# Performance work log

Measured on AMD Instinct MI355X. Metric: run time of the kernel, lower is better.

## Reference

```python
import jax, jax.numpy as jnp
import numpy as np

B, S, D, H = 2, 2048, 1024, 16
DK = D // H

def setup_inputs() -> dict:
    key = jax.random.key(0)
    ks = jax.random.split(key, 12)
    inp = {
        'Q': jax.random.normal(ks[0], (B, S, D), jnp.float32),
        'K': jax.random.normal(ks[1], (B, S, D), jnp.float32),
        'V': jax.random.normal(ks[2], (B, S, D), jnp.float32),
        # causal mask broadcast over batch/heads; masked_fill where mask==0
        'mask': jnp.tril(jnp.ones((1, 1, S, S), jnp.int32)),
        'Wq': jax.random.normal(ks[3], (D, D), jnp.float32) / np.sqrt(D),
        'bq': jnp.zeros((D,), jnp.float32),
        'Wk': jax.random.normal(ks[4], (D, D), jnp.float32) / np.sqrt(D),
        'bk': jnp.zeros((D,), jnp.float32),
        'Wv': jax.random.normal(ks[5], (D, D), jnp.float32) / np.sqrt(D),
        'bv': jnp.zeros((D,), jnp.float32),
        'Wo': jax.random.normal(ks[6], (D, D), jnp.float32) / np.sqrt(D),
        'bo': jnp.zeros((D,), jnp.float32),
    }
    return inp

def _split(x):
    # [B,S,D] -> [B,H,S,DK]
    return x.reshape(B, S, H, DK).transpose(0, 2, 1, 3)

def reference(Q, K, V, mask, Wq, bq, Wk, bk, Wv, bv, Wo, bo):
    q = _split(Q @ Wq.T + bq)
    k = _split(K @ Wk.T + bk)
    v = _split(V @ Wv.T + bv)
    score = jnp.einsum('bhqd,bhkd->bhqk', q, k) / jnp.sqrt(jnp.float32(DK))
    score = jnp.where(mask == 0, jnp.float32(-1e9), score)
    attn = jax.nn.softmax(score, axis=-1)  # dropout is identity at eval
    ctx = jnp.einsum('bhqk,bhkd->bhqd', attn, v)
    out = ctx.transpose(0, 2, 1, 3).reshape(B, S, D)
    return out @ Wo.T + bo
```

## Files before the change

### kernel.cpp

```cpp
#include <hip/hip_runtime.h>

#define B_  2
#define S_  2048
#define D_  1024
#define H_  16
#define DK_ 64

using bf16x8 = __attribute__((ext_vector_type(8))) short;
using f32x4  = __attribute__((ext_vector_type(4))) float;

__device__ __forceinline__ unsigned short f2bf(float f) {
    unsigned u = __builtin_bit_cast(unsigned, f);
    u += 0x7FFFu + ((u >> 16) & 1u);
    return (unsigned short)(u >> 16);
}

__device__ __forceinline__ void gload_lds16(const unsigned short* gsrc, unsigned short* ldst) {
    __builtin_amdgcn_global_load_lds((const __attribute__((address_space(1))) void*)gsrc,
                                     (__attribute__((address_space(3))) void*)ldst, 16, 0, 0);
}

__global__ __launch_bounds__(256) void cast_all_k(
    const float* __restrict__ Q, const float* __restrict__ K, const float* __restrict__ V,
    const float* __restrict__ Wq, const float* __restrict__ Wk, const float* __restrict__ Wv,
    const float* __restrict__ Wo, unsigned short* __restrict__ dst) {
    unsigned gid  = blockIdx.x * 256u + threadIdx.x;
    unsigned base = gid * 4u;
    unsigned seg  = base >> 20;
    const float* src; unsigned off;
    if      (seg <  4u) { src = Q;  off = base; }
    else if (seg <  8u) { src = K;  off = base - (4u  << 20); }
    else if (seg < 12u) { src = V;  off = base - (8u  << 20); }
    else if (seg == 12u){ src = Wq; off = base - (12u << 20); }
    else if (seg == 13u){ src = Wk; off = base - (13u << 20); }
    else if (seg == 14u){ src = Wv; off = base - (14u << 20); }
    else                { src = Wo; off = base - (15u << 20); }
    float4 v = *reinterpret_cast<const float4*>(src + off);
    ushort4 o;
    o.x = f2bf(v.x); o.y = f2bf(v.y); o.z = f2bf(v.z); o.w = f2bf(v.w);
    *reinterpret_cast<ushort4*>(dst + base) = o;
}

__device__ __forceinline__ void gemm_stage(
    const unsigned short* __restrict__ A, const unsigned short* __restrict__ Bm,
    int bm, int bn, int kt, unsigned short* As, unsigned short* Bs, int tid, int w) {
    #pragma unroll
    for (int is = 0; is < 2; ++is) {
        int g = is * 256 + tid;
        int row = g >> 2, c = g & 3;
        gload_lds16(A  + (unsigned)(bm * 128 + row) * 1024 + kt + c * 8,
                    As + (unsigned)(is * 256 + w * 64) * 8);
        gload_lds16(Bm + (unsigned)(bn * 128 + row) * 1024 + kt + c * 8,
                    Bs + (unsigned)(is * 256 + w * 64) * 8);
    }
}

__device__ __forceinline__ void gemm_core(
    const unsigned short* __restrict__ A, const unsigned short* __restrict__ Bm,
    int bm, int bn, f32x4 acc[4][4],
    unsigned short (&As)[2][128 * 32], unsigned short (&Bs)[2][128 * 32]) {
    const int tid = threadIdx.x;
    const int w = tid >> 6, l = tid & 63, lg = l >> 4, lr = l & 15;
    const int wr = w >> 1, wc = w & 1;
    gemm_stage(A, Bm, bm, bn, 0, As[0], Bs[0], tid, w);
    __syncthreads();
    for (int ks = 0; ks < 32; ++ks) {
        const int cur = ks & 1;
        if (ks + 1 < 32)
            gemm_stage(A, Bm, bm, bn, (ks + 1) * 32, As[cur ^ 1], Bs[cur ^ 1], tid, w);
        bf16x8 af[4], bfr[4];
        #pragma unroll
        for (int i = 0; i < 4; ++i)
            af[i]  = *reinterpret_cast<const bf16x8*>(&As[cur][(wr * 64 + i * 16 + lr) * 32 + lg * 8]);
        #pragma unroll
        for (int j = 0; j < 4; ++j)
            bfr[j] = *reinterpret_cast<const bf16x8*>(&Bs[cur][(wc * 64 + j * 16 + lr) * 32 + lg * 8]);
        #pragma unroll
        for (int i = 0; i < 4; ++i)
            #pragma unroll
            for (int j = 0; j < 4; ++j)
                acc[i][j] = __builtin_amdgcn_mfma_f32_16x16x32_bf16(af[i], bfr[j], acc[i][j], 0, 0, 0);
        __syncthreads();
    }
}

__global__ __launch_bounds__(256) void proj_fused_k(
    const unsigned short* __restrict__ bfall,
    const float* __restrict__ bq, const float* __restrict__ bk, const float* __restrict__ bv,
    unsigned short* __restrict__ qh, unsigned short* __restrict__ kh,
    unsigned short* __restrict__ vt) {
    __shared__ __align__(16) unsigned short As[2][128 * 32], Bs[2][128 * 32];
    const unsigned M1 = 1u << 20;
    int bid = blockIdx.x;
    int z = bid >> 8, r = bid & 255;
    const unsigned short *A, *Bm; const float* bias; unsigned short* outp;
    int bm, bn;
    if (z == 0)      { A = bfall;           Bm = bfall + 12 * M1; bias = bq; outp = qh; bm = r >> 3; bn = r & 7; }
    else if (z == 1) { A = bfall + 4 * M1;  Bm = bfall + 13 * M1; bias = bk; outp = kh; bm = r >> 3; bn = r & 7; }
    else             { A = bfall + 14 * M1; Bm = bfall + 8 * M1;  bias = bv; outp = vt; bm = r >> 5; bn = r & 31; }

    f32x4 acc[4][4] = {};
    gemm_core(A, Bm, bm, bn, acc, As, Bs);

    const int tid = threadIdx.x;
    const int w = tid >> 6, l = tid & 63, lg = l >> 4, lr = l & 15;
    const int wr = w >> 1, wc = w & 1;
    #pragma unroll
    for (int i = 0; i < 4; ++i) {
        #pragma unroll
        for (int j = 0; j < 4; ++j) {
            int n = bn * 128 + wc * 64 + j * 16 + lr;
            #pragma unroll
            for (int rr = 0; rr < 4; ++rr) {
                int m = bm * 128 + wr * 64 + i * 16 + 4 * lg + rr;
                float v = acc[i][j][rr];
                if (z < 2) {
                    v += bias[n];
                    if (z == 0) v *= 0.125f;
                    int b = m >> 11, s = m & 2047, h = n >> 6, d = n & 63;
                    outp[(((unsigned)(b * 16 + h) * 2048 + s) << 6) + d] = f2bf(v);
                } else {
                    v += bias[m];
                    int h = m >> 6, d = m & 63, b = n >> 11, s = n & 2047;
                    outp[(((unsigned)(b * 16 + h) << 6) + d) * 2048 + s] = f2bf(v);
                }
            }
        }
    }
}

__device__ __forceinline__ void attn_stage(
    const unsigned short* __restrict__ khb, const unsigned short* __restrict__ vtb,
    int kb, unsigned short* KtB, unsigned short* VtB, int tid, int w) {
    #pragma unroll
    for (int is = 0; is < 2; ++is) {
        int g = is * 256 + tid;
        int row = g >> 3, cp = g & 7;
        int ck = cp ^ (row & 7);
        gload_lds16(khb + (unsigned)(kb + row) * 64 + ck * 8,
                    KtB + (unsigned)(is * 256 + w * 64) * 8);
        gload_lds16(vtb + (unsigned)row * S_ + kb + ck * 8,
                    VtB + (unsigned)(is * 256 + w * 64) * 8);
    }
}

__global__ __launch_bounds__(256) void attn_k(
    const unsigned short* __restrict__ qh, const unsigned short* __restrict__ kh,
    const unsigned short* __restrict__ vt, unsigned short* __restrict__ ctx) {
    __shared__ __align__(16) unsigned short Kt[2][64 * 64], Vt[2][64 * 64], Pb[4][16 * 64];
    const int bh = blockIdx.x, qi = blockIdx.y;
    const int b = bh >> 4, h = bh & 15;
    const int qb = (S_ - 64) - 64 * qi;
    const int tid = threadIdx.x, w = tid >> 6, l = tid & 63, lg = l >> 4, lr = l & 15;
    const unsigned short* khb = kh + (unsigned)bh * S_ * 64;
    const unsigned short* vtb = vt + (unsigned)bh * 64 * S_;

    const unsigned short* qrow = qh + ((unsigned)bh * S_ + qb + w * 16 + lr) * 64 + lg * 8;
    const bf16x8 aq0 = *reinterpret_cast<const bf16x8*>(qrow);
    const bf16x8 aq1 = *reinterpret_cast<const bf16x8*>(qrow + 32);

    f32x4 o[4] = {};
    float m_r[4], l_r[4];
    #pragma unroll
    for (int rr = 0; rr < 4; ++rr) { m_r[rr] = -1e30f; l_r[rr] = 0.f; }

    const int ntiles = qb / 64 + 1;
    attn_stage(khb, vtb, 0, Kt[0], Vt[0], tid, w);
    __syncthreads();
    for (int t = 0; t < ntiles; ++t) {
        const int cur = t & 1;
        if (t + 1 < ntiles)
            attn_stage(khb, vtb, (t + 1) * 64, Kt[cur ^ 1], Vt[cur ^ 1], tid, w);
        const unsigned short* Kc = Kt[cur];
        const unsigned short* Vc = Vt[cur];

        f32x4 sf[4];
        __builtin_amdgcn_s_setprio(1);
        #pragma unroll
        for (int f = 0; f < 4; ++f) {
            f32x4 a = {};
            int row0 = f * 16 + lr;
            bf16x8 bk0 = *reinterpret_cast<const bf16x8*>(&Kc[row0 * 64 + ((lg + 0) ^ (row0 & 7)) * 8]);
            a = __builtin_amdgcn_mfma_f32_16x16x32_bf16(aq0, bk0, a, 0, 0, 0);
            bf16x8 bk1 = *reinterpret_cast<const bf16x8*>(&Kc[row0 * 64 + ((lg + 4) ^ (row0 & 7)) * 8]);
            a = __builtin_amdgcn_mfma_f32_16x16x32_bf16(aq1, bk1, a, 0, 0, 0);
            sf[f] = a;
        }
        __builtin_amdgcn_s_setprio(0);
        const bool diag = (t == ntiles - 1);
        float sc[4];
        #pragma unroll
        for (int rr = 0; rr < 4; ++rr) {
            float mv = -1e30f;
            #pragma unroll
            for (int f = 0; f < 4; ++f) {
                float v = sf[f][rr];
                if (diag && (f * 16 + lr) > (w * 16 + 4 * lg + rr)) v = -1e30f;
                sf[f][rr] = v;
                mv = fmaxf(mv, v);
            }
            mv = fmaxf(mv, __shfl_xor(mv, 1));
            mv = fmaxf(mv, __shfl_xor(mv, 2));
            mv = fmaxf(mv, __shfl_xor(mv, 4));
            mv = fmaxf(mv, __shfl_xor(mv, 8));
            float mn = fmaxf(m_r[rr], mv);
            sc[rr] = __expf(m_r[rr] - mn);
            m_r[rr] = mn;
            float s = 0.f;
            #pragma unroll
            for (int f = 0; f < 4; ++f) {
                float p = __expf(sf[f][rr] - mn);
                sf[f][rr] = p;
                s += p;
            }
            s += __shfl_xor(s, 1); s += __shfl_xor(s, 2);
            s += __shfl_xor(s, 4); s += __shfl_xor(s, 8);
            l_r[rr] = l_r[rr] * sc[rr] + s;
        }
        #pragma unroll
        for (int f2 = 0; f2 < 4; ++f2)
            #pragma unroll
            for (int rr = 0; rr < 4; ++rr)
                o[f2][rr] *= sc[rr];

        unsigned short* Pw = &Pb[w][0];
        #pragma unroll
        for (int f = 0; f < 4; ++f) {
            int col = f * 16 + lr, ch = col >> 3, wi = col & 7;
            #pragma unroll
            for (int rr = 0; rr < 4; ++rr) {
                int row = 4 * lg + rr;
                Pw[row * 64 + ((ch ^ (row & 7)) << 3) + wi] = f2bf(sf[f][rr]);
            }
        }
        asm volatile("s_waitcnt lgkmcnt(0)" ::: "memory");
        bf16x8 ap0 = *reinterpret_cast<const bf16x8*>(&Pw[lr * 64 + ((lg + 0) ^ (lr & 7)) * 8]);
        bf16x8 ap1 = *reinterpret_cast<const bf16x8*>(&Pw[lr * 64 + ((lg + 4) ^ (lr & 7)) * 8]);

        __builtin_amdgcn_s_setprio(1);
        #pragma unroll
        for (int f2 = 0; f2 < 4; ++f2) {
            int row = f2 * 16 + lr;
            bf16x8 bv0 = *reinterpret_cast<const bf16x8*>(&Vc[row * 64 + ((lg + 0) ^ (row & 7)) * 8]);
            o[f2] = __builtin_amdgcn_mfma_f32_16x16x32_bf16(ap0, bv0, o[f2], 0, 0, 0);
            bf16x8 bv1 = *reinterpret_cast<const bf16x8*>(&Vc[row * 64 + ((lg + 4) ^ (row & 7)) * 8]);
            o[f2] = __builtin_amdgcn_mfma_f32_16x16x32_bf16(ap1, bv1, o[f2], 0, 0, 0);
        }
        __builtin_amdgcn_s_setprio(0);
        __syncthreads();
    }

    #pragma unroll
    for (int f2 = 0; f2 < 4; ++f2) {
        #pragma unroll
        for (int rr = 0; rr < 4; ++rr) {
            int s = qb + w * 16 + 4 * lg + rr;
            float v = o[f2][rr] / l_r[rr];
            ctx[(((unsigned)(b * S_ + s) * H_ + h) << 6) + f2 * 16 + lr] = f2bf(v);
        }
    }
}

__global__ __launch_bounds__(256) void final_k(
    const unsigned short* __restrict__ ctx, const unsigned short* __restrict__ Wob,
    const float* __restrict__ bo, float* __restrict__ out) {
    __shared__ __align__(16) unsigned short As[2][128 * 32], Bs[2][128 * 32];
    int bid = blockIdx.x;
    int bm = bid >> 3, bn = bid & 7;
    f32x4 acc[4][4] = {};
    gemm_core(ctx, Wob, bm, bn, acc, As, Bs);
    const int tid = threadIdx.x;
    const int w = tid >> 6, l = tid & 63, lg = l >> 4, lr = l & 15;
    const int wr = w >> 1, wc = w & 1;
    #pragma unroll
    for (int i = 0; i < 4; ++i) {
        #pragma unroll
        for (int j = 0; j < 4; ++j) {
            int n = bn * 128 + wc * 64 + j * 16 + lr;
            float bn_v = bo[n];
            #pragma unroll
            for (int rr = 0; rr < 4; ++rr) {
                int m = bm * 128 + wr * 64 + i * 16 + 4 * lg + rr;
                out[(unsigned)m * 1024 + n] = acc[i][j][rr] + bn_v;
            }
        }
    }
}

extern "C" void kernel_launch(void* const* d_in, const int* in_sizes, int n_in,
                              void* d_out, int out_size, void* d_ws, size_t ws_size,
                              hipStream_t stream) {
    const float* Q  = (const float*)d_in[0];
    const float* K  = (const float*)d_in[1];
    const float* V  = (const float*)d_in[2];
    const float* Wq = (const float*)d_in[4];
    const float* bq = (const float*)d_in[5];
    const float* Wk = (const float*)d_in[6];
    const float* bk = (const float*)d_in[7];
    const float* Wv = (const float*)d_in[8];
    const float* bv = (const float*)d_in[9];
    const float* Wo = (const float*)d_in[10];
    const float* bo = (const float*)d_in[11];
    float* out = (float*)d_out;

    unsigned short* ws = (unsigned short*)d_ws;
    const unsigned M1 = 1u << 20;
    unsigned short* bfall = ws;
    unsigned short* qh    = ws + (size_t)16 * M1;
    unsigned short* khp   = ws + (size_t)20 * M1;
    unsigned short* vtp   = ws + (size_t)24 * M1;
    unsigned short* ctx   = ws;

    hipLaunchKernelGGL(cast_all_k, dim3(16384), dim3(256), 0, stream,
                       Q, K, V, Wq, Wk, Wv, Wo, bfall);
    hipLaunchKernelGGL(proj_fused_k, dim3(768), dim3(256), 0, stream,
                       bfall, bq, bk, bv, qh, khp, vtp);
    hipLaunchKernelGGL(attn_k, dim3(32, 32), dim3(256), 0, stream,
                       qh, khp, vtp, ctx);
    hipLaunchKernelGGL(final_k, dim3(256), dim3(256), 0, stream,
                       ctx, bfall + (size_t)15 * M1, bo, out);
}
```

Baseline: 267.3 us.

## Transpose attention MFMA operands, use exp2 softmax with lazy rescale, remap GEMM blocks

The attention kernel swaps the MFMA operand order so scores come out transposed. Each lane then owns a single query row, which removes most cross-lane max/sum shuffles and lets P and the output be written as packed bf16 via v_cvt_pk_bf16_f32. The Q scaling now folds in log2(e) so softmax can use the raw v_exp_f32 (exp2), and the running-max rescale is skipped when no row's max rises by more than a threshold. Block IDs in the projection and output GEMMs are also remapped so consecutive blocks spread across XCDs for better cache locality. The lazy rescale bounds unnormalized exponentials at about 2^11.5, which is safe in fp32 but relies on that threshold.

```diff
diff --git a/kernel.cpp b/kernel.cpp
--- a/kernel.cpp
+++ b/kernel.cpp
@@ -13,6 +13,18 @@
     unsigned u = __builtin_bit_cast(unsigned, f);
     u += 0x7FFFu + ((u >> 16) & 1u);
     return (unsigned short)(u >> 16);
+}
+
+__device__ __forceinline__ unsigned cvt_pk_bf16(float lo, float hi) {
+    unsigned r;
+    asm("v_cvt_pk_bf16_f32 %0, %1, %2" : "=v"(r) : "v"(lo), "v"(hi));
+    return r;
+}
+
+__device__ __forceinline__ float exp2_fast(float x) {
+    float r;
+    asm("v_exp_f32 %0, %1" : "=v"(r) : "v"(x));
+    return r;
 }
 
 __device__ __forceinline__ void gload_lds16(const unsigned short* gsrc, unsigned short* ldst) {
@@ -92,7 +104,8 @@
     __shared__ __align__(16) unsigned short As[2][128 * 32], Bs[2][128 * 32];
     const unsigned M1 = 1u << 20;
     int bid = blockIdx.x;
-    int z = bid >> 8, r = bid & 255;
+    int wgid = (bid & 7) * 96 + (bid >> 3);
+    int z = wgid >> 8, r = wgid & 255;
     const unsigned short *A, *Bm; const float* bias; unsigned short* outp;
     int bm, bn;
     if (z == 0)      { A = bfall;           Bm = bfall + 12 * M1; bias = bq; outp = qh; bm = r >> 3; bn = r & 7; }
@@ -116,7 +129,7 @@
                 float v = acc[i][j][rr];
                 if (z < 2) {
                     v += bias[n];
-                    if (z == 0) v *= 0.125f;
+                    if (z == 0) v *= 0.18033688f;
                     int b = m >> 11, s = m & 2047, h = n >> 6, d = n & 63;
                     outp[(((unsigned)(b * 16 + h) * 2048 + s) << 6) + d] = f2bf(v);
                 } else {
@@ -156,13 +169,12 @@
     const unsigned short* vtb = vt + (unsigned)bh * 64 * S_;
 
     const unsigned short* qrow = qh + ((unsigned)bh * S_ + qb + w * 16 + lr) * 64 + lg * 8;
-    const bf16x8 aq0 = *reinterpret_cast<const bf16x8*>(qrow);
-    const bf16x8 aq1 = *reinterpret_cast<const bf16x8*>(qrow + 32);
+    const bf16x8 bq0 = *reinterpret_cast<const bf16x8*>(qrow);
+    const bf16x8 bq1 = *reinterpret_cast<const bf16x8*>(qrow + 32);
 
     f32x4 o[4] = {};
-    float m_r[4], l_r[4];
-    #pragma unroll
-    for (int rr = 0; rr < 4; ++rr) { m_r[rr] = -1e30f; l_r[rr] = 0.f; }
+    float m_r = -1e30f, l_r = 0.f;
+    const int swz = (lr & 7) << 4;
 
     const int ntiles = qb / 64 + 1;
     attn_stage(khb, vtb, 0, Kt[0], Vt[0], tid, w);
@@ -180,84 +192,87 @@
         for (int f = 0; f < 4; ++f) {
             f32x4 a = {};
             int row0 = f * 16 + lr;
-            bf16x8 bk0 = *reinterpret_cast<const bf16x8*>(&Kc[row0 * 64 + ((lg + 0) ^ (row0 & 7)) * 8]);
-            a = __builtin_amdgcn_mfma_f32_16x16x32_bf16(aq0, bk0, a, 0, 0, 0);
-            bf16x8 bk1 = *reinterpret_cast<const bf16x8*>(&Kc[row0 * 64 + ((lg + 4) ^ (row0 & 7)) * 8]);
-            a = __builtin_amdgcn_mfma_f32_16x16x32_bf16(aq1, bk1, a, 0, 0, 0);
+            bf16x8 ak0 = *reinterpret_cast<const bf16x8*>(&Kc[row0 * 64 + ((lg + 0) ^ (row0 & 7)) * 8]);
+            a = __builtin_amdgcn_mfma_f32_16x16x32_bf16(ak0, bq0, a, 0, 0, 0);
+            bf16x8 ak1 = *reinterpret_cast<const bf16x8*>(&Kc[row0 * 64 + ((lg + 4) ^ (row0 & 7)) * 8]);
+            a = __builtin_amdgcn_mfma_f32_16x16x32_bf16(ak1, bq1, a, 0, 0, 0);
             sf[f] = a;
         }
         __builtin_amdgcn_s_setprio(0);
-        const bool diag = (t == ntiles - 1);
-        float sc[4];
-        #pragma unroll
-        for (int rr = 0; rr < 4; ++rr) {
-            float mv = -1e30f;
-            #pragma unroll
-            for (int f = 0; f < 4; ++f) {
-                float v = sf[f][rr];
-                if (diag && (f * 16 + lr) > (w * 16 + 4 * lg + rr)) v = -1e30f;
-                sf[f][rr] = v;
-                mv = fmaxf(mv, v);
-            }
-            mv = fmaxf(mv, __shfl_xor(mv, 1));
-            mv = fmaxf(mv, __shfl_xor(mv, 2));
-            mv = fmaxf(mv, __shfl_xor(mv, 4));
-            mv = fmaxf(mv, __shfl_xor(mv, 8));
-            float mn = fmaxf(m_r[rr], mv);
-            sc[rr] = __expf(m_r[rr] - mn);
-            m_r[rr] = mn;
-            float s = 0.f;
-            #pragma unroll
-            for (int f = 0; f < 4; ++f) {
-                float p = __expf(sf[f][rr] - mn);
+
+        if (t == ntiles - 1) {
+            #pragma unroll
+            for (int f = 0; f < 4; ++f)
+                #pragma unroll
+                for (int rr = 0; rr < 4; ++rr)
+                    if (16 * f + 4 * lg + rr > w * 16 + lr) sf[f][rr] = -1e30f;
+        }
+        float pmax = -1e30f;
+        #pragma unroll
+        for (int f = 0; f < 4; ++f)
+            #pragma unroll
+            for (int rr = 0; rr < 4; ++rr)
+                pmax = fmaxf(pmax, sf[f][rr]);
+        pmax = fmaxf(pmax, __shfl_xor(pmax, 16));
+        pmax = fmaxf(pmax, __shfl_xor(pmax, 32));
+        if (!__all(pmax <= m_r + 11.5f)) {
+            float mn = fmaxf(m_r, pmax);
+            float sc = exp2_fast(m_r - mn);
+            #pragma unroll
+            for (int f2 = 0; f2 < 4; ++f2)
+                #pragma unroll
+                for (int rr = 0; rr < 4; ++rr)
+                    o[f2][rr] *= sc;
+            l_r *= sc;
+            m_r = mn;
+        }
+        float s = 0.f;
+        #pragma unroll
+        for (int f = 0; f < 4; ++f)
+            #pragma unroll
+            for (int rr = 0; rr < 4; ++rr) {
+                float p = exp2_fast(sf[f][rr] - m_r);
                 sf[f][rr] = p;
                 s += p;
             }
-            s += __shfl_xor(s, 1); s += __shfl_xor(s, 2);
-            s += __shfl_xor(s, 4); s += __shfl_xor(s, 8);
-            l_r[rr] = l_r[rr] * sc[rr] + s;
-        }
-        #pragma unroll
-        for (int f2 = 0; f2 < 4; ++f2)
-            #pragma unroll
-            for (int rr = 0; rr < 4; ++rr)
-                o[f2][rr] *= sc[rr];
-
-        unsigned short* Pw = &Pb[w][0];
+        s += __shfl_xor(s, 16);
+        s += __shfl_xor(s, 32);
+        l_r += s;
+
+        char* Pw = (char*)&Pb[w][0];
         #pragma unroll
         for (int f = 0; f < 4; ++f) {
-            int col = f * 16 + lr, ch = col >> 3, wi = col & 7;
-            #pragma unroll
-            for (int rr = 0; rr < 4; ++rr) {
-                int row = 4 * lg + rr;
-                Pw[row * 64 + ((ch ^ (row & 7)) << 3) + wi] = f2bf(sf[f][rr]);
-            }
+            uint2 u;
+            u.x = cvt_pk_bf16(sf[f][0], sf[f][1]);
+            u.y = cvt_pk_bf16(sf[f][2], sf[f][3]);
+            *reinterpret_cast<uint2*>(Pw + lr * 128 + ((32 * f + 8 * lg) ^ swz)) = u;
         }
         asm volatile("s_waitcnt lgkmcnt(0)" ::: "memory");
-        bf16x8 ap0 = *reinterpret_cast<const bf16x8*>(&Pw[lr * 64 + ((lg + 0) ^ (lr & 7)) * 8]);
-        bf16x8 ap1 = *reinterpret_cast<const bf16x8*>(&Pw[lr * 64 + ((lg + 4) ^ (lr & 7)) * 8]);
+        bf16x8 bp0 = *reinterpret_cast<const bf16x8*>(Pw + lr * 128 + ((16 * lg) ^ swz));
+        bf16x8 bp1 = *reinterpret_cast<const bf16x8*>(Pw + lr * 128 + ((64 + 16 * lg) ^ swz));
 
         __builtin_amdgcn_s_setprio(1);
         #pragma unroll
         for (int f2 = 0; f2 < 4; ++f2) {
             int row = f2 * 16 + lr;
-            bf16x8 bv0 = *reinterpret_cast<const bf16x8*>(&Vc[row * 64 + ((lg + 0) ^ (row & 7)) * 8]);
-            o[f2] = __builtin_amdgcn_mfma_f32_16x16x32_bf16(ap0, bv0, o[f2], 0, 0, 0);
-            bf16x8 bv1 = *reinterpret_cast<const bf16x8*>(&Vc[row * 64 + ((lg + 4) ^ (row & 7)) * 8]);
-            o[f2] = __builtin_amdgcn_mfma_f32_16x16x32_bf16(ap1, bv1, o[f2], 0, 0, 0);
+            bf16x8 av0 = *reinterpret_cast<const bf16x8*>(&Vc[row * 64 + ((lg + 0) ^ (row & 7)) * 8]);
+            o[f2] = __builtin_amdgcn_mfma_f32_16x16x32_bf16(av0, bp0, o[f2], 0, 0, 0);
+            bf16x8 av1 = *reinterpret_cast<const bf16x8*>(&Vc[row * 64 + ((lg + 4) ^ (row & 7)) * 8]);
+            o[f2] = __builtin_amdgcn_mfma_f32_16x16x32_bf16(av1, bp1, o[f2], 0, 0, 0);
         }
         __builtin_amdgcn_s_setprio(0);
         __syncthreads();
     }
 
+    const float inv = 1.f / l_r;
+    const int s_row = qb + w * 16 + lr;
+    unsigned short* cbase = ctx + (((unsigned)(b * S_ + s_row) * H_ + h) << 6);
     #pragma unroll
     for (int f2 = 0; f2 < 4; ++f2) {
-        #pragma unroll
-        for (int rr = 0; rr < 4; ++rr) {
-            int s = qb + w * 16 + 4 * lg + rr;
-            float v = o[f2][rr] / l_r[rr];
-            ctx[(((unsigned)(b * S_ + s) * H_ + h) << 6) + f2 * 16 + lr] = f2bf(v);
-        }
+        uint2 u;
+        u.x = cvt_pk_bf16(o[f2][0] * inv, o[f2][1] * inv);
+        u.y = cvt_pk_bf16(o[f2][2] * inv, o[f2][3] * inv);
+        *reinterpret_cast<uint2*>(cbase + f2 * 16 + lg * 4) = u;
     }
 }
 
@@ -266,7 +281,8 @@
     const float* __restrict__ bo, float* __restrict__ out) {
     __shared__ __align__(16) unsigned short As[2][128 * 32], Bs[2][128 * 32];
     int bid = blockIdx.x;
-    int bm = bid >> 3, bn = bid & 7;
+    int wgid = (bid & 7) * 32 + (bid >> 3);
+    int bm = wgid >> 3, bn = wgid & 7;
     f32x4 acc[4][4] = {};
     gemm_core(ctx, Wob, bm, bn, acc, As, Bs);
     const int tid = threadIdx.x;
```

New measurement: 246.3 us. -7.9%, faster.
